# Performance work log

Measured on AMD Instinct MI355X. Metric: run time of the kernel, lower is better.

Reference implementation:

```python
import jax, jax.numpy as jnp
import numpy as np

B, TS, TT = 32, 128, 64
V_SRC, V_TRG, E, H = 30000, 30000, 256, 512


def _cell(x, h, c, Wih, Whh, b):
    # x:[B,in], h,c:[B,H]; PyTorch gate order i,f,g,o
    g = x @ Wih.T + h @ Whh.T + b
    i, f, gg, o = jnp.split(g, 4, axis=-1)
    c = jax.nn.sigmoid(f) * c + jax.nn.sigmoid(i) * jnp.tanh(gg)
    h = jax.nn.sigmoid(o) * jnp.tanh(c)
    return h, c


def _lstm2(xs, p0, p1, state):
    # xs: [T,B,in]; 2-layer LSTM (dropout disabled / eval mode)
    def step(carry, x):
        h0, c0, h1, c1 = carry
        h0, c0 = _cell(x, h0, c0, *p0)
        h1, c1 = _cell(h0, h1, c1, *p1)
        return (h0, c0, h1, c1), h1
    carry, ys = jax.lax.scan(step, state, xs)
    return ys, carry


def setup_inputs() -> dict:
    key = jax.random.key(0)
    ks = jax.random.split(key, 28)
    n = lambda k, s: jax.random.normal(k, s, dtype=jnp.float32) * 0.05
    inp = {
        'src': jax.random.randint(ks[0], (B, TS), 0, V_SRC),
        'trg': jax.random.randint(ks[1], (B, TT), 0, V_TRG),
        'enc_emb': n(ks[2], (V_SRC, E)),
        'dec_emb': n(ks[3], (V_TRG, E)),
        'enc_Wih0': n(ks[4], (4 * H, E)), 'enc_Whh0': n(ks[5], (4 * H, H)),
        'enc_b0': n(ks[6], (4 * H,)),
        'enc_Wih1': n(ks[7], (4 * H, H)), 'enc_Whh1': n(ks[8], (4 * H, H)),
        'enc_b1': n(ks[9], (4 * H,)),
        'dec_Wih0': n(ks[10], (4 * H, E)), 'dec_Whh0': n(ks[11], (4 * H, H)),
        'dec_b0': n(ks[12], (4 * H,)),
        'dec_Wih1': n(ks[13], (4 * H, H)), 'dec_Whh1': n(ks[14], (4 * H, H)),
        'dec_b1': n(ks[15], (4 * H,)),
        'fc_W': n(ks[16], (V_TRG, H)), 'fc_b': n(ks[17], (V_TRG,)),
    }
    return inp


def reference(src, trg, enc_emb, dec_emb,
              enc_Wih0, enc_Whh0, enc_b0, enc_Wih1, enc_Whh1, enc_b1,
              dec_Wih0, dec_Whh0, dec_b0, dec_Wih1, dec_Whh1, dec_b1,
              fc_W, fc_b):
    zero = jnp.zeros((B, H), dtype=jnp.float32)
    # ---- Encoder ----
    src_e = enc_emb[src]                       # [B,TS,E]
    _, enc_state = _lstm2(jnp.swapaxes(src_e, 0, 1),
                          (enc_Wih0, enc_Whh0, enc_b0),
                          (enc_Wih1, enc_Whh1, enc_b1),
                          (zero, zero, zero, zero))
    # ---- Decoder (teacher forcing = 1.0): inputs trg[:, :-1] ----
    dec_in = dec_emb[trg[:, :-1]]              # [B,TT-1,E]
    hs, _ = _lstm2(jnp.swapaxes(dec_in, 0, 1),
                   (dec_Wih0, dec_Whh0, dec_b0),
                   (dec_Wih1, dec_Whh1, dec_b1),
                   enc_state)                  # hs: [TT-1,B,H]
    logits = jnp.einsum('tbh,vh->btv', hs, fc_W) + fc_b  # [B,TT-1,V]
    # outputs[:,0,:] stays zero as in original
    out = jnp.concatenate([jnp.zeros((B, 1, V_TRG), dtype=jnp.float32), logits], axis=1)
    return out
```

## Files before the change

### kernel.cpp

```cpp
#include <hip/hip_runtime.h>
#include <hip/hip_bf16.h>

#define B_SZ 32
#define TS 128
#define TT 64
#define TD 63
#define E_DIM 256
#define H_DIM 512
#define G4 2048
#define V_TRG 30000
#define NWG_L 32

typedef __attribute__((ext_vector_type(8))) short s8v;
typedef __attribute__((ext_vector_type(4))) float f32x4;
typedef unsigned short u16;
typedef unsigned int u32;
typedef unsigned long long u64;

static __device__ __forceinline__ float sigf(float x) {
  x = fminf(fmaxf(x, -30.f), 30.f);
  return 1.0f / (1.0f + __expf(-x));
}
static __device__ __forceinline__ float tanh_(float x) {
  x = fminf(fmaxf(x, -15.f), 15.f);
  float e = __expf(2.0f * x);
  return (e - 1.0f) / (e + 1.0f);
}
static __device__ __forceinline__ u16 f2bf(float x) {
  union { float f; unsigned u; } v; v.f = x;
  unsigned r = v.u + 0x7FFF + ((v.u >> 16) & 1);
  return (u16)(r >> 16);
}

struct Cvt { const float* s; u16* d; int n; };
struct Cvt9 { Cvt m[9]; };

__global__ void cvt_kernel(Cvt9 c) {
  const Cvt cv = c.m[blockIdx.y];
  int i = blockIdx.x * 256 + threadIdx.x;
  const int stride = gridDim.x * 256;
  for (; i < cv.n; i += stride) cv.d[i] = f2bf(cv.s[i]);
}

__global__ void embed_kernel(const int* __restrict__ tok, const float* __restrict__ emb,
                             u16* __restrict__ x, int rows, int tstride) {
  int i = blockIdx.x * 256 + threadIdx.x;
  if (i >= rows * E_DIM) return;
  int e = i & (E_DIM - 1);
  int r = i >> 8;
  int b = r & 31, t = r >> 5;
  int token = tok[b * tstride + t];
  x[i] = f2bf(emb[token * E_DIM + e]);
}

template<int MODE>
__global__ __launch_bounds__(256) void gemm_bf16(
    const u16* __restrict__ A, const u16* __restrict__ Bw,
    const float* __restrict__ bias, float* __restrict__ out,
    int M, int N, int K) {
  __shared__ u16 As[128 * 40];
  __shared__ u16 Bs[128 * 40];
  const int nb = blockIdx.x, mb = blockIdx.y;
  const int tid = threadIdx.x;
  const int w = tid >> 6, lane = tid & 63, quad = lane >> 4, cc = lane & 15;
  const int wm = w & 1, wn = w >> 1;
  f32x4 acc[4][4] = {};

  for (int k0 = 0; k0 < K; k0 += 32) {
    #pragma unroll
    for (int i = tid; i < 512; i += 256) {
      int m = i >> 2, kk = (i & 3) << 3;
      int gm = mb * 128 + m;
      s8v va = {};
      if (gm < M) va = *(const s8v*)(A + (size_t)gm * K + k0 + kk);
      *(s8v*)(&As[m * 40 + kk]) = va;
      int gn = nb * 128 + m;
      s8v vb = {};
      if (gn < N) vb = *(const s8v*)(Bw + (size_t)gn * K + k0 + kk);
      *(s8v*)(&Bs[m * 40 + kk]) = vb;
    }
    __syncthreads();
    s8v af[4], bf[4];
    #pragma unroll
    for (int mt = 0; mt < 4; ++mt)
      af[mt] = *(const s8v*)(&As[(wm * 64 + mt * 16 + cc) * 40 + quad * 8]);
    #pragma unroll
    for (int nt = 0; nt < 4; ++nt)
      bf[nt] = *(const s8v*)(&Bs[(wn * 64 + nt * 16 + cc) * 40 + quad * 8]);
    #pragma unroll
    for (int mt = 0; mt < 4; ++mt)
      #pragma unroll
      for (int nt = 0; nt < 4; ++nt)
        acc[mt][nt] = __builtin_amdgcn_mfma_f32_16x16x32_bf16(af[mt], bf[nt], acc[mt][nt], 0, 0, 0);
    __syncthreads();
  }

  #pragma unroll
  for (int mt = 0; mt < 4; ++mt)
    #pragma unroll
    for (int nt = 0; nt < 4; ++nt) {
      int col = nb * 128 + wn * 64 + nt * 16 + cc;
      if (col >= N) continue;
      float bv = bias[col];
      #pragma unroll
      for (int r = 0; r < 4; ++r) {
        int row = mb * 128 + wm * 64 + mt * 16 + quad * 4 + r;
        if (row >= M) continue;
        float v = acc[mt][nt][r] + bv;
        if (MODE == 0) {
          out[(size_t)row * N + col] = v;
        } else {
          int t = row >> 5, b = row & 31;
          out[(size_t)b * (TT * V_TRG) + (size_t)(t + 1) * V_TRG + col] = v;
        }
      }
    }
}

union PK { u32 w[4]; s8v v; };

static __device__ __forceinline__ void poll16(const u32* __restrict__ base, u32 tag, PK* a) {
  const u64 tp  = (u64)tag | ((u64)tag << 32);
  const u64 MSK = 0x0000FFFF0000FFFFULL;
  for (;;) {
    u64 bad = 0;
    #pragma unroll
    for (int ks = 0; ks < 16; ++ks) {
      const u64* p = (const u64*)(base + ks * 32);
      #pragma unroll
      for (int i = 0; i < 4; ++i) {
        u64 q = __hip_atomic_load(p + i, __ATOMIC_RELAXED, __HIP_MEMORY_SCOPE_AGENT);
        bad |= (q ^ tp) & MSK;
        a[ks].w[i] = (u32)(((q >> 16) & 0xFFFFULL) | ((q >> 32) & 0xFFFF0000ULL));
      }
    }
    if (!__any(bad != 0)) return;
    __builtin_amdgcn_s_sleep(2);
  }
}

__global__ __launch_bounds__(128, 1) void lstm2_scan(
    const u16* __restrict__ X,
    const u16* __restrict__ Wih0,
    const u16* __restrict__ Whh0,
    const float* __restrict__ bias0,
    const u16* __restrict__ Wih1,
    const u16* __restrict__ Whh1,
    const float* __restrict__ bias1,
    const u16* __restrict__ h0i, const float* __restrict__ c0i,
    const u16* __restrict__ h1i, const float* __restrict__ c1i,
    u32* __restrict__ H0x,
    u32* __restrict__ H1x,
    u16* __restrict__ Hplain,
    u16* __restrict__ h0f, float* __restrict__ c0f,
    u16* __restrict__ h1f, float* __restrict__ c1f,
    int T) {
  __shared__ u16 BsH[64 * 512];
  __shared__ u16 BsX[64 * 512];
  const bool L1 = (blockIdx.x >= NWG_L);
  const int jn = blockIdx.x & 31;
  const int tid = threadIdx.x;
  const int mt = tid >> 6, lane = tid & 63, quad = lane >> 4, cc = lane & 15;

  {
    const u16* Wh = L1 ? Whh1 : Whh0;
    for (int i = tid; i < 64 * 64; i += 128) {
      int col = i >> 6, kc = i & 63;
      int row = (col >> 4) * 512 + jn * 16 + (col & 15);
      s8v v = *(const s8v*)(Wh + (size_t)row * 512 + kc * 8);
      *(s8v*)(&BsH[col * 512 + ((kc + col) & 63) * 8]) = v;
    }
    if (L1) {
      for (int i = tid; i < 64 * 64; i += 128) {
        int col = i >> 6, kc = i & 63;
        int row = (col >> 4) * 512 + jn * 16 + (col & 15);
        s8v v = *(const s8v*)(Wih1 + (size_t)row * 512 + kc * 8);
        *(s8v*)(&BsX[col * 512 + ((kc + col) & 63) * 8]) = v;
      }
    } else {
      for (int i = tid; i < 64 * 32; i += 128) {
        int col = i >> 5, kc = i & 31;
        int row = (col >> 4) * 512 + jn * 16 + (col & 15);
        s8v v = *(const s8v*)(Wih0 + (size_t)row * 256 + kc * 8);
        *(s8v*)(&BsX[col * 256 + ((kc + col) & 31) * 8]) = v;
      }
    }
  }
  __syncthreads();

  const int br = mt * 16 + quad * 4;
  const int j  = jn * 16 + cc;
  const int arow = (mt * 16 + cc) * H_DIM + quad * 8;

  const float* biasp = L1 ? bias1 : bias0;
  float bv4[4];
  #pragma unroll
  for (int g = 0; g < 4; ++g) bv4[g] = biasp[g * 512 + j];

  f32x4 creg;
  {
    const float* ci = L1 ? c1i : c0i;
    #pragma unroll
    for (int r = 0; r < 4; ++r) creg[r] = ci[(br + r) * H_DIM + j];
  }

  PK a[16];

  if (!L1) {
    for (int s = 0; s < T; ++s) {
      f32x4 acc[4] = {};
      const u16* xrow = X + ((size_t)(s * B_SZ) + mt * 16 + cc) * E_DIM + quad * 8;
      #pragma unroll
      for (int ks = 0; ks < 8; ++ks) {
        s8v xa = *(const s8v*)(xrow + ks * 32);
        int kc = ks * 4 + quad;
        #pragma unroll
        for (int g = 0; g < 4; ++g) {
          int col = g * 16 + cc;
          s8v bx = *(const s8v*)(&BsX[col * 256 + ((kc + col) & 31) * 8]);
          acc[g] = __builtin_amdgcn_mfma_f32_16x16x32_bf16(xa, bx, acc[g], 0, 0, 0);
        }
      }
      if (s == 0) {
        #pragma unroll
        for (int ks = 0; ks < 16; ++ks)
          a[ks].v = *(const s8v*)(h0i + arow + ks * 32);
      } else {
        poll16(H0x + (size_t)(s - 1) * (B_SZ * H_DIM) + arow, (u32)s, a);
      }
      #pragma unroll
      for (int ks = 0; ks < 16; ++ks) {
        int kc = ks * 4 + quad;
        #pragma unroll
        for (int g = 0; g < 4; ++g) {
          int col = g * 16 + cc;
          s8v bh = *(const s8v*)(&BsH[col * 512 + ((kc + col) & 63) * 8]);
          acc[g] = __builtin_amdgcn_mfma_f32_16x16x32_bf16(a[ks].v, bh, acc[g], 0, 0, 0);
        }
      }
      u32* hw = H0x + (size_t)s * (B_SZ * H_DIM);
      const u32 tg = (u32)(s + 1);
      #pragma unroll
      for (int r = 0; r < 4; ++r) {
        float gi = acc[0][r] + bv4[0];
        float gf = acc[1][r] + bv4[1];
        float gg = acc[2][r] + bv4[2];
        float go = acc[3][r] + bv4[3];
        float cn = sigf(gf) * creg[r] + sigf(gi) * tanh_(gg);
        float hn = sigf(go) * tanh_(cn);
        creg[r] = cn;
        u16 hb = f2bf(hn);
        __hip_atomic_store(&hw[(br + r) * H_DIM + j], ((u32)hb << 16) | tg,
                           __ATOMIC_RELAXED, __HIP_MEMORY_SCOPE_AGENT);
        if (s == T - 1 && h0f) {
          h0f[(br + r) * H_DIM + j] = hb;
          c0f[(br + r) * H_DIM + j] = cn;
        }
      }
    }
  } else {
    for (int s = 0; s < T; ++s) {
      f32x4 acc[4] = {};
      poll16(H0x + (size_t)s * (B_SZ * H_DIM) + arow, (u32)(s + 1), a);
      #pragma unroll
      for (int ks = 0; ks < 16; ++ks) {
        int kc = ks * 4 + quad;
        #pragma unroll
        for (int g = 0; g < 4; ++g) {
          int col = g * 16 + cc;
          s8v bx = *(const s8v*)(&BsX[col * 512 + ((kc + col) & 63) * 8]);
          acc[g] = __builtin_amdgcn_mfma_f32_16x16x32_bf16(a[ks].v, bx, acc[g], 0, 0, 0);
        }
      }
      if (s == 0) {
        #pragma unroll
        for (int ks = 0; ks < 16; ++ks)
          a[ks].v = *(const s8v*)(h1i + arow + ks * 32);
      } else {
        poll16(H1x + (size_t)(s - 1) * (B_SZ * H_DIM) + arow, (u32)s, a);
      }
      #pragma unroll
      for (int ks = 0; ks < 16; ++ks) {
        int kc = ks * 4 + quad;
        #pragma unroll
        for (int g = 0; g < 4; ++g) {
          int col = g * 16 + cc;
          s8v bh = *(const s8v*)(&BsH[col * 512 + ((kc + col) & 63) * 8]);
          acc[g] = __builtin_amdgcn_mfma_f32_16x16x32_bf16(a[ks].v, bh, acc[g], 0, 0, 0);
        }
      }
      u32* hw = H1x + (size_t)s * (B_SZ * H_DIM);
      const u32 tg = (u32)(s + 1);
      #pragma unroll
      for (int r = 0; r < 4; ++r) {
        float gi = acc[0][r] + bv4[0];
        float gf = acc[1][r] + bv4[1];
        float gg = acc[2][r] + bv4[2];
        float go = acc[3][r] + bv4[3];
        float cn = sigf(gf) * creg[r] + sigf(gi) * tanh_(gg);
        float hn = sigf(go) * tanh_(cn);
        creg[r] = cn;
        u16 hb = f2bf(hn);
        __hip_atomic_store(&hw[(br + r) * H_DIM + j], ((u32)hb << 16) | tg,
                           __ATOMIC_RELAXED, __HIP_MEMORY_SCOPE_AGENT);
        if (Hplain)
          Hplain[(size_t)(s * B_SZ + br + r) * H_DIM + j] = hb;
        if (s == T - 1 && h1f) {
          h1f[(br + r) * H_DIM + j] = hb;
          c1f[(br + r) * H_DIM + j] = cn;
        }
      }
    }
  }
}

__global__ void zero_t0_kernel(float* __restrict__ out) {
  int i = blockIdx.x * 256 + threadIdx.x;
  if (i >= B_SZ * V_TRG) return;
  int b = i / V_TRG, v = i - b * V_TRG;
  out[(size_t)b * (TT * V_TRG) + v] = 0.f;
}

extern "C" void kernel_launch(void* const* d_in, const int* in_sizes, int n_in,
                              void* d_out, int out_size, void* d_ws, size_t ws_size,
                              hipStream_t stream) {
  const int*   src     = (const int*)d_in[0];
  const int*   trg     = (const int*)d_in[1];
  const float* enc_emb = (const float*)d_in[2];
  const float* dec_emb = (const float*)d_in[3];
  const float* eW0i = (const float*)d_in[4];
  const float* eW0h = (const float*)d_in[5];
  const float* eb0  = (const float*)d_in[6];
  const float* eW1i = (const float*)d_in[7];
  const float* eW1h = (const float*)d_in[8];
  const float* eb1  = (const float*)d_in[9];
  const float* dW0i = (const float*)d_in[10];
  const float* dW0h = (const float*)d_in[11];
  const float* db0  = (const float*)d_in[12];
  const float* dW1i = (const float*)d_in[13];
  const float* dW1h = (const float*)d_in[14];
  const float* db1  = (const float*)d_in[15];
  const float* fcW  = (const float*)d_in[16];
  const float* fcb  = (const float*)d_in[17];
  float* out = (float*)d_out;

  char* ws = (char*)d_ws;
  size_t off = 0;
  auto alloc = [&](size_t bytes) {
    char* p = ws + off;
    off = (off + bytes + 255) & ~(size_t)255;
    return p;
  };
  u16*   hzero  = (u16*)alloc(B_SZ * H_DIM * 2);
  float* czero  = (float*)alloc(B_SZ * H_DIM * 4);
  u16* eW0i_b = (u16*)alloc((size_t)G4 * E_DIM * 2);
  u16* eW0h_b = (u16*)alloc((size_t)G4 * H_DIM * 2);
  u16* eW1i_b = (u16*)alloc((size_t)G4 * H_DIM * 2);
  u16* eW1h_b = (u16*)alloc((size_t)G4 * H_DIM * 2);
  u16* dW0i_b = (u16*)alloc((size_t)G4 * E_DIM * 2);
  u16* dW0h_b = (u16*)alloc((size_t)G4 * H_DIM * 2);
  u16* dW1i_b = (u16*)alloc((size_t)G4 * H_DIM * 2);
  u16* dW1h_b = (u16*)alloc((size_t)G4 * H_DIM * 2);
  u16* fcW_b  = (u16*)alloc((size_t)V_TRG * H_DIM * 2);
  u16* x_enc  = (u16*)alloc((size_t)TS * B_SZ * E_DIM * 2);
  u16* x_dec  = (u16*)alloc((size_t)TD * B_SZ * E_DIM * 2);
  const size_t PLANE_E = (size_t)TS * B_SZ * H_DIM;
  const size_t PLANE_D = (size_t)TD * B_SZ * H_DIM;
  u32* tagbase = (u32*)alloc((2 * PLANE_E + 2 * PLANE_D) * 4);
  u32* H0e = tagbase;
  u32* H1e = H0e + PLANE_E;
  u32* H0d = H1e + PLANE_E;
  u32* H1d = H0d + PLANE_D;
  u16* H1d_p  = (u16*)alloc((size_t)TD * B_SZ * H_DIM * 2);
  u16* hF0    = (u16*)alloc(B_SZ * H_DIM * 2);
  float* cF0  = (float*)alloc(B_SZ * H_DIM * 4);
  u16* hF1    = (u16*)alloc(B_SZ * H_DIM * 2);
  float* cF1  = (float*)alloc(B_SZ * H_DIM * 4);

  hipMemsetAsync(hzero, 0, B_SZ * H_DIM * 2, stream);
  hipMemsetAsync(czero, 0, B_SZ * H_DIM * 4, stream);
  hipMemsetAsync(tagbase, 0, (2 * PLANE_E + 2 * PLANE_D) * 4, stream);

  Cvt9 c9 = {{ {eW0i, eW0i_b, G4 * E_DIM}, {eW0h, eW0h_b, G4 * H_DIM},
               {eW1i, eW1i_b, G4 * H_DIM}, {eW1h, eW1h_b, G4 * H_DIM},
               {dW0i, dW0i_b, G4 * E_DIM}, {dW0h, dW0h_b, G4 * H_DIM},
               {dW1i, dW1i_b, G4 * H_DIM}, {dW1h, dW1h_b, G4 * H_DIM},
               {fcW,  fcW_b,  V_TRG * H_DIM} }};
  cvt_kernel<<<dim3(1024, 9), 256, 0, stream>>>(c9);

  embed_kernel<<<(TS * B_SZ * E_DIM + 255) / 256, 256, 0, stream>>>(src, enc_emb, x_enc, TS * B_SZ, TS);
  embed_kernel<<<(TD * B_SZ * E_DIM + 255) / 256, 256, 0, stream>>>(trg, dec_emb, x_dec, TD * B_SZ, TT);

  lstm2_scan<<<2 * NWG_L, 128, 0, stream>>>(
      x_enc, eW0i_b, eW0h_b, eb0, eW1i_b, eW1h_b, eb1,
      hzero, czero, hzero, czero,
      H0e, H1e, (u16*)nullptr,
      hF0, cF0, hF1, cF1, TS);

  lstm2_scan<<<2 * NWG_L, 128, 0, stream>>>(
      x_dec, dW0i_b, dW0h_b, db0, dW1i_b, dW1h_b, db1,
      hF0, cF0, hF1, cF1,
      H0d, H1d, H1d_p,
      (u16*)nullptr, (float*)nullptr, (u16*)nullptr, (float*)nullptr, TD);

  gemm_bf16<1><<<dim3((V_TRG + 127) / 128, (TD * B_SZ + 127) / 128), 256, 0, stream>>>(
      H1d_p, fcW_b, fcb, out, TD * B_SZ, V_TRG, H_DIM);
  zero_t0_kernel<<<(B_SZ * V_TRG + 255) / 256, 256, 0, stream>>>(out);
}
```

Baseline: 2.185 ms.

## Issue hidden-state loads before MFMA work and reorder layer-1 dependency waits

The polling of tagged hidden states is split into an up-front volley of atomic loads, issued before independent MFMA work, and a later check that re-polls only the 16-byte chunks whose tags are stale. Layer 1 now consumes its own previous hidden state first and waits on layer 0's current output only afterwards, so the recurrent matmul runs while layer 0 finishes. Byte packing uses a perm instruction. This costs more registers for the 64 in-flight u64 loads and can hit stale data more often, which triggers per-chunk re-polling.

New measurement: 4.430 ms. +102.7%, slower.

```diff
diff --git a/kernel.cpp b/kernel.cpp
--- a/kernel.cpp
+++ b/kernel.cpp
@@ -119,23 +119,48 @@
 
 union PK { u32 w[4]; s8v v; };
 
-static __device__ __forceinline__ void poll16(const u32* __restrict__ base, u32 tag, PK* a) {
+#define ALD(p) __hip_atomic_load((p), __ATOMIC_RELAXED, __HIP_MEMORY_SCOPE_AGENT)
+
+static __device__ __forceinline__ void volley16(const u32* __restrict__ base, u64 q[16][4]) {
+  #pragma unroll
+  for (int ks = 0; ks < 16; ++ks) {
+    const u64* p = (const u64*)(base + ks * 32);
+    #pragma unroll
+    for (int i = 0; i < 4; ++i) q[ks][i] = ALD(p + i);
+  }
+}
+
+static __device__ __forceinline__ u32 pk(u64 q) {
+  return __builtin_amdgcn_perm((u32)(q >> 32), (u32)q, 0x07060302);
+}
+
+static __device__ __forceinline__ void packfix16(const u32* __restrict__ base, u32 tag,
+                                                 u64 q[16][4], PK* a) {
   const u64 tp  = (u64)tag | ((u64)tag << 32);
   const u64 MSK = 0x0000FFFF0000FFFFULL;
-  for (;;) {
+  unsigned badm = 0;
+  #pragma unroll
+  for (int ks = 0; ks < 16; ++ks) {
     u64 bad = 0;
     #pragma unroll
-    for (int ks = 0; ks < 16; ++ks) {
-      const u64* p = (const u64*)(base + ks * 32);
-      #pragma unroll
-      for (int i = 0; i < 4; ++i) {
-        u64 q = __hip_atomic_load(p + i, __ATOMIC_RELAXED, __HIP_MEMORY_SCOPE_AGENT);
-        bad |= (q ^ tp) & MSK;
-        a[ks].w[i] = (u32)(((q >> 16) & 0xFFFFULL) | ((q >> 32) & 0xFFFF0000ULL));
-      }
-    }
-    if (!__any(bad != 0)) return;
-    __builtin_amdgcn_s_sleep(2);
+    for (int i = 0; i < 4; ++i) bad |= (q[ks][i] ^ tp) & MSK;
+    badm |= (bad != 0 ? 1u : 0u) << ks;
+    #pragma unroll
+    for (int i = 0; i < 4; ++i) a[ks].w[i] = pk(q[ks][i]);
+  }
+  while (__builtin_expect(badm != 0, 0)) {
+    int ks = __builtin_ctz(badm);
+    const u64* p = (const u64*)(base + ks * 32);
+    u64 qq[4]; u64 bad;
+    do {
+      bad = 0;
+      #pragma unroll
+      for (int i = 0; i < 4; ++i) { qq[i] = ALD(p + i); bad |= (qq[i] ^ tp) & MSK; }
+      if (bad) __builtin_amdgcn_s_sleep(1);
+    } while (bad != 0);
+    #pragma unroll
+    for (int i = 0; i < 4; ++i) a[ks].w[i] = pk(qq[i]);
+    badm &= badm - 1;
   }
 }
 
@@ -204,29 +229,35 @@
     for (int r = 0; r < 4; ++r) creg[r] = ci[(br + r) * H_DIM + j];
   }
 
-  PK a[16];
-
   if (!L1) {
     for (int s = 0; s < T; ++s) {
+      const u16* xrow = X + ((size_t)(s * B_SZ) + mt * 16 + cc) * E_DIM + quad * 8;
+      s8v xa[8];
+      #pragma unroll
+      for (int ks = 0; ks < 8; ++ks) xa[ks] = *(const s8v*)(xrow + ks * 32);
+
+      u64 q[16][4];
+      const u32* hb = H0x + (size_t)(s - 1) * (B_SZ * H_DIM) + arow;
+      if (s > 0) volley16(hb, q);
+
       f32x4 acc[4] = {};
-      const u16* xrow = X + ((size_t)(s * B_SZ) + mt * 16 + cc) * E_DIM + quad * 8;
       #pragma unroll
       for (int ks = 0; ks < 8; ++ks) {
-        s8v xa = *(const s8v*)(xrow + ks * 32);
         int kc = ks * 4 + quad;
         #pragma unroll
         for (int g = 0; g < 4; ++g) {
           int col = g * 16 + cc;
           s8v bx = *(const s8v*)(&BsX[col * 256 + ((kc + col) & 31) * 8]);
-          acc[g] = __builtin_amdgcn_mfma_f32_16x16x32_bf16(xa, bx, acc[g], 0, 0, 0);
-        }
-      }
-      if (s == 0) {
-        #pragma unroll
-        for (int ks = 0; ks < 16; ++ks)
-          a[ks].v = *(const s8v*)(h0i + arow + ks * 32);
+          acc[g] = __builtin_amdgcn_mfma_f32_16x16x32_bf16(xa[ks], bx, acc[g], 0, 0, 0);
+        }
+      }
+
+      PK a[16];
+      if (s > 0) {
+        packfix16(hb, (u32)s, q, a);
       } else {
-        poll16(H0x + (size_t)(s - 1) * (B_SZ * H_DIM) + arow, (u32)s, a);
+        #pragma unroll
+        for (int ks = 0; ks < 16; ++ks) a[ks].v = *(const s8v*)(h0i + arow + ks * 32);
       }
       #pragma unroll
       for (int ks = 0; ks < 16; ++ks) {
@@ -238,6 +269,7 @@
           acc[g] = __builtin_amdgcn_mfma_f32_16x16x32_bf16(a[ks].v, bh, acc[g], 0, 0, 0);
         }
       }
+
       u32* hw = H0x + (size_t)s * (B_SZ * H_DIM);
       const u32 tg = (u32)(s + 1);
       #pragma unroll
@@ -249,19 +281,44 @@
         float cn = sigf(gf) * creg[r] + sigf(gi) * tanh_(gg);
         float hn = sigf(go) * tanh_(cn);
         creg[r] = cn;
-        u16 hb = f2bf(hn);
-        __hip_atomic_store(&hw[(br + r) * H_DIM + j], ((u32)hb << 16) | tg,
+        u16 hb2 = f2bf(hn);
+        __hip_atomic_store(&hw[(br + r) * H_DIM + j], ((u32)hb2 << 16) | tg,
                            __ATOMIC_RELAXED, __HIP_MEMORY_SCOPE_AGENT);
         if (s == T - 1 && h0f) {
-          h0f[(br + r) * H_DIM + j] = hb;
+          h0f[(br + r) * H_DIM + j] = hb2;
           c0f[(br + r) * H_DIM + j] = cn;
         }
       }
     }
   } else {
     for (int s = 0; s < T; ++s) {
+      u64 q[16][4];
+      PK a[16];
+      if (s > 0) {
+        const u32* hb1 = H1x + (size_t)(s - 1) * (B_SZ * H_DIM) + arow;
+        volley16(hb1, q);
+        packfix16(hb1, (u32)s, q, a);
+      } else {
+        #pragma unroll
+        for (int ks = 0; ks < 16; ++ks) a[ks].v = *(const s8v*)(h1i + arow + ks * 32);
+      }
+
+      const u32* hb0 = H0x + (size_t)s * (B_SZ * H_DIM) + arow;
+      volley16(hb0, q);
+
       f32x4 acc[4] = {};
-      poll16(H0x + (size_t)s * (B_SZ * H_DIM) + arow, (u32)(s + 1), a);
+      #pragma unroll
+      for (int ks = 0; ks < 16; ++ks) {
+        int kc = ks * 4 + quad;
+        #pragma unroll
+        for (int g = 0; g < 4; ++g) {
+          int col = g * 16 + cc;
+          s8v bh = *(const s8v*)(&BsH[col * 512 + ((kc + col) & 63) * 8]);
+          acc[g] = __builtin_amdgcn_mfma_f32_16x16x32_bf16(a[ks].v, bh, acc[g], 0, 0, 0);
+        }
+      }
+
+      packfix16(hb0, (u32)(s + 1), q, a);
       #pragma unroll
       for (int ks = 0; ks < 16; ++ks) {
         int kc = ks * 4 + quad;
@@ -272,23 +329,7 @@
           acc[g] = __builtin_amdgcn_mfma_f32_16x16x32_bf16(a[ks].v, bx, acc[g], 0, 0, 0);
         }
       }
-      if (s == 0) {
-        #pragma unroll
-        for (int ks = 0; ks < 16; ++ks)
-          a[ks].v = *(const s8v*)(h1i + arow + ks * 32);
-      } else {
-        poll16(H1x + (size_t)(s - 1) * (B_SZ * H_DIM) + arow, (u32)s, a);
-      }
-      #pragma unroll
-      for (int ks = 0; ks < 16; ++ks) {
-        int kc = ks * 4 + quad;
-        #pragma unroll
-        for (int g = 0; g < 4; ++g) {
-          int col = g * 16 + cc;
-          s8v bh = *(const s8v*)(&BsH[col * 512 + ((kc + col) & 63) * 8]);
-          acc[g] = __builtin_amdgcn_mfma_f32_16x16x32_bf16(a[ks].v, bh, acc[g], 0, 0, 0);
-        }
-      }
+
       u32* hw = H1x + (size_t)s * (B_SZ * H_DIM);
       const u32 tg = (u32)(s + 1);
       #pragma unroll
@@ -300,13 +341,13 @@
         float cn = sigf(gf) * creg[r] + sigf(gi) * tanh_(gg);
         float hn = sigf(go) * tanh_(cn);
         creg[r] = cn;
-        u16 hb = f2bf(hn);
-        __hip_atomic_store(&hw[(br + r) * H_DIM + j], ((u32)hb << 16) | tg,
+        u16 hb2 = f2bf(hn);
+        __hip_atomic_store(&hw[(br + r) * H_DIM + j], ((u32)hb2 << 16) | tg,
                            __ATOMIC_RELAXED, __HIP_MEMORY_SCOPE_AGENT);
         if (Hplain)
-          Hplain[(size_t)(s * B_SZ + br + r) * H_DIM + j] = hb;
+          Hplain[(size_t)(s * B_SZ + br + r) * H_DIM + j] = hb2;
         if (s == T - 1 && h1f) {
-          h1f[(br + r) * H_DIM + j] = hb;
+          h1f[(br + r) * H_DIM + j] = hb2;
           c1f[(br + r) * H_DIM + j] = cn;
         }
       }
```
